# Optimization experiments

Hardware: AMD Instinct MI355X
Metric: run time of the kernel (lower is better)

Reference implementation:

```python
import jax, jax.numpy as jnp
import numpy as np


def setup_inputs() -> dict:
    key = jax.random.key(0)
    k1, k2 = jax.random.split(key)
    N, C = 16384, 4096
    x = jax.random.normal(k1, (N, C), dtype=jnp.float32)
    y = jax.random.randint(k2, (N, C), 0, 2, dtype=jnp.int64)
    return {"x": x, "y": y}


def reference(x, y):
    # Original loss: for each row i,
    #   loss_i = 1/(ni*(C-ni)) * sum_{j: y=1, k: y=0} exp(-(x_k - x_j))
    # which factorizes exactly into separable masked row sums:
    #   loss_i = (sum_{y=1} exp(x)) * (sum_{y=0} exp(-x)) / (ni*(C-ni))
    C = x.shape[1]
    m = (y == 1)
    pos = jnp.sum(jnp.where(m, jnp.exp(x), 0.0), axis=1)   # sum exp(x) over y==1
    neg = jnp.sum(jnp.where(m, 0.0, jnp.exp(-x)), axis=1)  # sum exp(-x) over y==0
    ni = jnp.sum(m, axis=1).astype(x.dtype)
    loss = jnp.mean(pos * neg / (ni * (C - ni)))
    return loss
```

## Files before the change

### kernel.cpp

```cpp
#include <hip/hip_runtime.h>


#define C_DIM 4096
#define BLOCK 256
#define WPB   (BLOCK / 64)

__global__ __launch_bounds__(BLOCK) void pdl_rows(const float* __restrict__ x,
                                                  const int* __restrict__ y,
                                                  float* __restrict__ partial) {
    const int lane = threadIdx.x & 63;
    const int wave = threadIdx.x >> 6;
    const int row  = blockIdx.x * WPB + wave;

    const float4* __restrict__ x4 = (const float4*)(x + (size_t)row * C_DIM);
    const int4*  __restrict__ y4 = (const int4*)(y + (size_t)row * C_DIM);

    float pos = 0.0f, neg = 0.0f;
    int cnt = 0;

    float4 xa[4], xb[4];
    int4  ya[4], yb[4];

    auto prefetch = [&](float4 (&xv)[4], int4 (&yv)[4], int c) {
#pragma unroll
        for (int u = 0; u < 4; ++u) {
            const int i = lane + (c * 4 + u) * 64;
            xv[u] = x4[i];
            yv[u] = y4[i];
        }
    };
    auto compute = [&](const float4 (&xv)[4], const int4 (&yv)[4]) {
#pragma unroll
        for (int u = 0; u < 4; ++u) {
            { const float e = __expf(yv[u].x ? xv[u].x : -xv[u].x);
              pos += yv[u].x ? e : 0.0f; neg += yv[u].x ? 0.0f : e; cnt += yv[u].x; }
            { const float e = __expf(yv[u].y ? xv[u].y : -xv[u].y);
              pos += yv[u].y ? e : 0.0f; neg += yv[u].y ? 0.0f : e; cnt += yv[u].y; }
            { const float e = __expf(yv[u].z ? xv[u].z : -xv[u].z);
              pos += yv[u].z ? e : 0.0f; neg += yv[u].z ? 0.0f : e; cnt += yv[u].z; }
            { const float e = __expf(yv[u].w ? xv[u].w : -xv[u].w);
              pos += yv[u].w ? e : 0.0f; neg += yv[u].w ? 0.0f : e; cnt += yv[u].w; }
        }
    };

    prefetch(xa, ya, 0);
    prefetch(xb, yb, 1);
    compute(xa, ya);
    prefetch(xa, ya, 2);
    compute(xb, yb);
    prefetch(xb, yb, 3);
    compute(xa, ya);
    compute(xb, yb);

#pragma unroll
    for (int off = 32; off >= 1; off >>= 1) {
        pos += __shfl_down(pos, off, 64);
        neg += __shfl_down(neg, off, 64);
        cnt += __shfl_down(cnt, off, 64);
    }

    __shared__ float sacc[WPB];
    if (lane == 0) {
        const float denom = (float)cnt * (float)(C_DIM - cnt);
        sacc[wave] = (pos * neg) / denom;
    }
    __syncthreads();
    if (threadIdx.x == 0) {
        float b = 0.0f;
#pragma unroll
        for (int w = 0; w < WPB; ++w) b += sacc[w];
        partial[blockIdx.x] = b;
    }
}

__global__ __launch_bounds__(BLOCK) void pdl_reduce(const float* __restrict__ partial,
                                                    float* __restrict__ out,
                                                    int n_partial, float inv_n) {
    const float4* p4 = (const float4*)partial;
    float s = 0.0f;
    for (int i = threadIdx.x; i < n_partial / 4; i += BLOCK) {
        const float4 v = p4[i];
        s += (v.x + v.y) + (v.z + v.w);
    }
#pragma unroll
    for (int off = 32; off >= 1; off >>= 1) s += __shfl_down(s, off, 64);
    __shared__ float sw[WPB];
    const int lane = threadIdx.x & 63;
    const int wave = threadIdx.x >> 6;
    if (lane == 0) sw[wave] = s;
    __syncthreads();
    if (threadIdx.x == 0) {
        float t = 0.0f;
#pragma unroll
        for (int w = 0; w < WPB; ++w) t += sw[w];
        out[0] = t * inv_n;
    }
}

extern "C" void kernel_launch(void* const* d_in, const int* in_sizes, int n_in,
                              void* d_out, int out_size, void* d_ws, size_t ws_size,
                              hipStream_t stream) {
    const float* x = (const float*)d_in[0];
    const int*   y = (const int*)d_in[1];
    float* out = (float*)d_out;
    float* partial = (float*)d_ws;

    const int n_rows  = in_sizes[0] / C_DIM;
    const int n_blocks = n_rows / WPB;

    pdl_rows<<<n_blocks, BLOCK, 0, stream>>>(x, y, partial);
    pdl_reduce<<<1, BLOCK, 0, stream>>>(partial, out, n_blocks, 1.0f / (float)n_rows);
}
```

Measured before the change: 498.2 us.

## Route label loads through LDS via global_load_lds with four-stage nontemporal x pipeline

Labels are now loaded directly into LDS with global_load_lds, while x is read into registers with nontemporal inline-asm loads. A four-slot software pipeline with explicit vmcnt waits keeps up to four chunks in flight per wave. The aim is to raise memory-level parallelism and cut VGPR pressure on this bandwidth-bound streaming reduction. It adds LDS use and hand-written waitcnt logic that is fragile and could serialize if the counts are wrong. The grid size is also hardcoded to 4096 blocks.

```diff
diff --git a/kernel.cpp b/kernel.cpp
--- a/kernel.cpp
+++ b/kernel.cpp
@@ -1,56 +1,103 @@
 #include <hip/hip_runtime.h>
+#include <stdint.h>
 
+
+typedef float    v4f __attribute__((ext_vector_type(4)));
+typedef unsigned v4u __attribute__((ext_vector_type(4)));
 
 #define C_DIM 4096
 #define BLOCK 256
-#define WPB   (BLOCK / 64)
+#define WPB   4
+#define NBLK  4096
+
+typedef __attribute__((address_space(1))) const void gvoid;
+typedef __attribute__((address_space(3))) void lvoid;
 
 __global__ __launch_bounds__(BLOCK) void pdl_rows(const float* __restrict__ x,
                                                   const int* __restrict__ y,
                                                   float* __restrict__ partial) {
+    __shared__ v4u yslots[WPB][4][2][64];
+    __shared__ float sacc[WPB];
+
     const int lane = threadIdx.x & 63;
     const int wave = threadIdx.x >> 6;
     const int row  = blockIdx.x * WPB + wave;
 
-    const float4* __restrict__ x4 = (const float4*)(x + (size_t)row * C_DIM);
-    const int4*  __restrict__ y4 = (const int4*)(y + (size_t)row * C_DIM);
+    const v4f* xp = (const v4f*)(x + (size_t)row * C_DIM) + lane;
+    const v4u* yp = (const v4u*)(y + (size_t)row * C_DIM) + lane;
 
+    const unsigned lds_rd =
+        (unsigned)(size_t)(__attribute__((address_space(3))) char*)&yslots[wave][0][0][0]
+        + (unsigned)lane * 16u;
+
+    v4f xs0[4], xs1[4];
     float pos = 0.0f, neg = 0.0f;
     int cnt = 0;
 
-    float4 xa[4], xb[4];
-    int4  ya[4], yb[4];
+#define ISSUE(s, c)                                                           \
+    do {                                                                      \
+        const v4f* pa0 = xp + ((c) * 2 + 0) * 64;                             \
+        const v4f* pa1 = xp + ((c) * 2 + 1) * 64;                             \
+        asm volatile("global_load_dwordx4 %0, %1, off nt"                     \
+                     : "=v"(xs0[s]) : "v"(pa0) : "memory");                   \
+        asm volatile("global_load_dwordx4 %0, %1, off nt"                     \
+                     : "=v"(xs1[s]) : "v"(pa1) : "memory");                   \
+        __builtin_amdgcn_global_load_lds((gvoid*)(yp + ((c) * 2 + 0) * 64),   \
+                                         (lvoid*)&yslots[wave][s][0][0],      \
+                                         16, 0, 0);                           \
+        __builtin_amdgcn_global_load_lds((gvoid*)(yp + ((c) * 2 + 1) * 64),   \
+                                         (lvoid*)&yslots[wave][s][1][0],      \
+                                         16, 0, 0);                           \
+    } while (0)
 
-    auto prefetch = [&](float4 (&xv)[4], int4 (&yv)[4], int c) {
-#pragma unroll
-        for (int u = 0; u < 4; ++u) {
-            const int i = lane + (c * 4 + u) * 64;
-            xv[u] = x4[i];
-            yv[u] = y4[i];
-        }
-    };
-    auto compute = [&](const float4 (&xv)[4], const int4 (&yv)[4]) {
-#pragma unroll
-        for (int u = 0; u < 4; ++u) {
-            { const float e = __expf(yv[u].x ? xv[u].x : -xv[u].x);
-              pos += yv[u].x ? e : 0.0f; neg += yv[u].x ? 0.0f : e; cnt += yv[u].x; }
-            { const float e = __expf(yv[u].y ? xv[u].y : -xv[u].y);
-              pos += yv[u].y ? e : 0.0f; neg += yv[u].y ? 0.0f : e; cnt += yv[u].y; }
-            { const float e = __expf(yv[u].z ? xv[u].z : -xv[u].z);
-              pos += yv[u].z ? e : 0.0f; neg += yv[u].z ? 0.0f : e; cnt += yv[u].z; }
-            { const float e = __expf(yv[u].w ? xv[u].w : -xv[u].w);
-              pos += yv[u].w ? e : 0.0f; neg += yv[u].w ? 0.0f : e; cnt += yv[u].w; }
-        }
-    };
+#define CONSUME(s, N, yv0, yv1)                                               \
+    asm volatile("s_waitcnt vmcnt(" #N ")\n\t"                                \
+                 "ds_read_b128 %0, %4 offset:0\n\t"                           \
+                 "ds_read_b128 %1, %4 offset:1024\n\t"                        \
+                 "s_waitcnt lgkmcnt(0)"                                       \
+                 : "=&v"(yv0), "=&v"(yv1), "+v"(xs0[s]), "+v"(xs1[s])         \
+                 : "v"(lds_rd + (s) * 2048u) : "memory")
 
-    prefetch(xa, ya, 0);
-    prefetch(xb, yb, 1);
-    compute(xa, ya);
-    prefetch(xa, ya, 2);
-    compute(xb, yb);
-    prefetch(xb, yb, 3);
-    compute(xa, ya);
-    compute(xb, yb);
+#define COMPUTE(t0, t1, yv0, yv1)                                             \
+    do {                                                                      \
+        _Pragma("unroll")                                                     \
+        for (int e = 0; e < 4; ++e) {                                         \
+            { const unsigned yy = yv0[e]; const float xx = t0[e];             \
+              const float ex = __expf(yy ? xx : -xx);                         \
+              pos += yy ? ex : 0.0f; neg += yy ? 0.0f : ex; cnt += (int)yy; } \
+            { const unsigned yy = yv1[e]; const float xx = t1[e];             \
+              const float ex = __expf(yy ? xx : -xx);                         \
+              pos += yy ? ex : 0.0f; neg += yy ? 0.0f : ex; cnt += (int)yy; } \
+        }                                                                     \
+    } while (0)
+
+#define ITER_ISSUE(c, s, N)                                                   \
+    do {                                                                      \
+        v4u yv0, yv1;                                                         \
+        CONSUME(s, N, yv0, yv1);                                              \
+        const v4f t0 = xs0[s], t1 = xs1[s];                                   \
+        ISSUE(s, (c) + 4);                                                    \
+        COMPUTE(t0, t1, yv0, yv1);                                            \
+    } while (0)
+
+#define ITER_TAIL(c, s, N)                                                    \
+    do {                                                                      \
+        v4u yv0, yv1;                                                         \
+        CONSUME(s, N, yv0, yv1);                                              \
+        const v4f t0 = xs0[s], t1 = xs1[s];                                   \
+        COMPUTE(t0, t1, yv0, yv1);                                            \
+    } while (0)
+
+    ISSUE(0, 0); ISSUE(1, 1); ISSUE(2, 2); ISSUE(3, 3);
+
+    ITER_ISSUE(0, 0, 12);
+    ITER_ISSUE(1, 1, 12);
+    ITER_ISSUE(2, 2, 12);
+    ITER_ISSUE(3, 3, 12);
+    ITER_TAIL (4, 0, 12);
+    ITER_TAIL (5, 1, 8);
+    ITER_TAIL (6, 2, 4);
+    ITER_TAIL (7, 3, 0);
 
 #pragma unroll
     for (int off = 32; off >= 1; off >>= 1) {
@@ -59,7 +106,6 @@
         cnt += __shfl_down(cnt, off, 64);
     }
 
-    __shared__ float sacc[WPB];
     if (lane == 0) {
         const float denom = (float)cnt * (float)(C_DIM - cnt);
         sacc[wave] = (pos * neg) / denom;
@@ -84,7 +130,7 @@
     }
 #pragma unroll
     for (int off = 32; off >= 1; off >>= 1) s += __shfl_down(s, off, 64);
-    __shared__ float sw[WPB];
+    __shared__ float sw[BLOCK / 64];
     const int lane = threadIdx.x & 63;
     const int wave = threadIdx.x >> 6;
     if (lane == 0) sw[wave] = s;
@@ -92,7 +138,7 @@
     if (threadIdx.x == 0) {
         float t = 0.0f;
 #pragma unroll
-        for (int w = 0; w < WPB; ++w) t += sw[w];
+        for (int w = 0; w < BLOCK / 64; ++w) t += sw[w];
         out[0] = t * inv_n;
     }
 }
@@ -105,9 +151,8 @@
     float* out = (float*)d_out;
     float* partial = (float*)d_ws;
 
-    const int n_rows  = in_sizes[0] / C_DIM;
-    const int n_blocks = n_rows / WPB;
+    const int n_rows = in_sizes[0] / C_DIM;
 
-    pdl_rows<<<n_blocks, BLOCK, 0, stream>>>(x, y, partial);
-    pdl_reduce<<<1, BLOCK, 0, stream>>>(partial, out, n_blocks, 1.0f / (float)n_rows);
+    pdl_rows<<<NBLK, BLOCK, 0, stream>>>(x, y, partial);
+    pdl_reduce<<<1, BLOCK, 0, stream>>>(partial, out, NBLK, 1.0f / (float)n_rows);
 }
```

After: 491.5 us. Within noise of the previous version (-1.4%).
